# Optimization experiments

Hardware: AMD Instinct MI355X
Metric: run time of the kernel (lower is better)

The kernel has to match this reference:

```python
import jax, jax.numpy as jnp
import numpy as np

NE = 256          # number of electrons
D = 256           # attention_dim = num_heads * heads_dim
H = 4             # num_heads
DH = 64           # heads_dim
L = 2             # num_layers
NDETS = 1
MASK_LEN = 0.1


def _ln(x, s, b):
    m = jnp.mean(x, -1, keepdims=True)
    v = jnp.var(x, -1, keepdims=True)
    return (x - m) * jax.lax.rsqrt(v + 1e-5) * s + b


def setup_inputs() -> dict:
    key = jax.random.key(0)
    ks = jax.random.split(key, 16)
    n = lambda k, sh, sc: (jax.random.normal(k, sh) * sc).astype(jnp.float32)
    theta = jax.random.uniform(ks[0], (NE,), minval=0.1, maxval=np.pi - 0.1)
    phi = jax.random.uniform(ks[1], (NE,), minval=0.0, maxval=2.0 * np.pi)
    return {
        "electrons": jnp.stack([theta, phi], -1).astype(jnp.float32),
        "W_in": n(ks[2], (3, D), 3 ** -0.5),
        "Wq": n(ks[3], (L, D, H, DH), D ** -0.5),
        "bq": jnp.zeros((L, H, DH), jnp.float32),
        "Wk": n(ks[4], (L, D, H, DH), D ** -0.5),
        "bk": jnp.zeros((L, H, DH), jnp.float32),
        "Wv": n(ks[5], (L, D, H, DH), D ** -0.5),
        "bv": jnp.zeros((L, H, DH), jnp.float32),
        "Wo": n(ks[6], (L, H, DH, D), D ** -0.5),
        "bo": jnp.zeros((L, D), jnp.float32),
        "W1": n(ks[7], (L, D, D), D ** -0.5),
        "ln1_s": jnp.ones((L, D), jnp.float32),
        "ln1_b": jnp.zeros((L, D), jnp.float32),
        "W2": n(ks[8], (L, D, D), D ** -0.5),
        "b2": jnp.zeros((L, D), jnp.float32),
        "ln2_s": jnp.ones((L, D), jnp.float32),
        "ln2_b": jnp.zeros((L, D), jnp.float32),
        "Worb_r": n(ks[9], (D, NDETS * 2), D ** -0.5),
        "Worb_i": n(ks[10], (D, NDETS * 2), D ** -0.5),
    }


def reference(electrons, W_in, Wq, bq, Wk, bk, Wv, bv, Wo, bo, W1, ln1_s, ln1_b,
              W2, b2, ln2_s, ln2_b, Worb_r, Worb_i):
    theta, phi = electrons[..., 0], electrons[..., 1]
    # ---- pair gather: P = NE*(NE-1)/2 unordered pairs ----
    iu, ju = jnp.triu_indices(NE, k=1)
    th_p = jnp.stack([theta[iu], theta[ju]], -1)   # [P, 2]
    ph_p = jnp.stack([phi[iu], phi[ju]], -1)       # [P, 2]
    # input_feature: (cos t, sin t cos p, sin t sin p)
    feat = jnp.stack([jnp.cos(th_p), jnp.sin(th_p) * jnp.cos(ph_p),
                      jnp.sin(th_p) * jnp.sin(ph_p)], -1)  # [P, 2, 3]
    # ---- batched mini-transformer over all pairs (seq len 2) ----
    h = feat @ W_in  # [P, 2, D]
    for l in range(L):
        q = jnp.einsum('psd,dhk->pshk', h, Wq[l]) + bq[l]
        k = jnp.einsum('psd,dhk->pshk', h, Wk[l]) + bk[l]
        v = jnp.einsum('psd,dhk->pshk', h, Wv[l]) + bv[l]
        logits = jnp.einsum('pshk,pthk->phst', q / np.sqrt(DH), k)
        attn = jax.nn.softmax(logits, axis=-1)
        o = jnp.einsum('phst,pthk->pshk', attn, v)
        mha = jnp.einsum('pshk,hkd->psd', o, Wo[l]) + bo[l]
        h = h + mha @ W1[l]
        h = _ln(h, ln1_s[l], ln1_b[l])
        h = h + jnp.tanh(h @ W2[l] + b2[l])
        h = _ln(h, ln2_s[l], ln2_b[l])
    # ---- pair orbitals: complex dense -> [P, ndets, 2 elec, 2 orb] ----
    orb = (h @ Worb_r + 1j * (h @ Worb_i)).astype(jnp.complex64)  # [P, 2, ndets*2]
    orb = orb.reshape(-1, 2, NDETS, 2).transpose(0, 2, 1, 3)      # [P, ndets, 2, 2]
    # ---- pairwise truncation factor ----
    u = jnp.cos(th_p / 2) * jnp.exp(1j * ph_p / 2)   # [P, 2]
    v_ = jnp.sin(th_p / 2) * jnp.exp(-1j * ph_p / 2)
    chord = jnp.abs(u[:, 0] * v_[:, 1] - u[:, 1] * v_[:, 0])
    trunc = 1.0 - jnp.exp(-(chord / MASK_LEN) ** 2)  # [P]
    orb = orb * trunc[:, None, None, None]
    dets = jnp.linalg.det(orb)          # [P, ndets]
    pair_orbs = jnp.sum(dets, axis=-1)  # [P]
    # ---- scatter into antisymmetric NE x NE matrix ----
    pf = jnp.zeros((NE, NE), jnp.complex64).at[iu, ju].set(pair_orbs)
    pf = pf - pf.T
    # ---- cusp matrix ----
    ue = jnp.cos(theta / 2) * jnp.exp(0.5j * phi)   # [NE]
    ve = jnp.sin(theta / 2) * jnp.exp(-0.5j * phi)
    elem = ue[:, None] * ve[None, :] - ve[:, None] * ue[None, :]  # [NE, NE]
    eye = jnp.eye(NE, dtype=jnp.float32)
    elem_c = elem + eye
    rho_c = jnp.abs(elem_c)
    cusp = elem_c * jnp.exp(-(rho_c / MASK_LEN) ** 2)
    # ---- pfaffian = sqrt(det), in log space for stability ----
    sign, logabs = jnp.linalg.slogdet(pf + cusp)
    log_ferm = 0.5 * (logabs.astype(jnp.complex64) + 1j * jnp.angle(sign))
    # ---- bosonic flux attachment (truncated product), in log space ----
    rho = jnp.abs(elem)
    masked = jnp.sqrt(MASK_LEN ** 2 + rho ** 2) * elem / (rho + eye) + eye
    log_bos = jnp.sum(jnp.log(masked.astype(jnp.complex64)))
    return log_ferm + log_bos
```

## Files before the change

kernel.cpp:

```cpp
#include <hip/hip_runtime.h>
#include <math.h>
#include <stdint.h>

#define NE 256
#define DD 256
#define NL 2
#define P_TOT 32640
#define NCHUNK 3
#define PC (P_TOT / NCHUNK)
#define MC (2 * PC)
#define MT (MC / 128)
#define NB 32
#define NPANEL (NE / NB)

typedef __bf16 bf16x8 __attribute__((ext_vector_type(8)));
typedef float f32x4 __attribute__((ext_vector_type(4)));

__device__ __forceinline__ float bf2f(ushort h) {
    union { unsigned u; float f; } c; c.u = ((unsigned)h) << 16; return c.f;
}
__device__ __forceinline__ ushort f2bf(float f) {
    union { float f; unsigned u; } c; c.f = f;
    unsigned u = c.u;
    return (ushort)((u + 0x7fffu + ((u >> 16) & 1u)) >> 16);
}

#define GLD16(gp, lp) __builtin_amdgcn_global_load_lds( \
    (const __attribute__((address_space(1))) unsigned int*)(uintptr_t)(gp), \
    (__attribute__((address_space(3))) unsigned int*)(uintptr_t)(lp), 16, 0, 0)

__global__ void idx_k(int* __restrict__ ip, int* __restrict__ jp) {
    int i = threadIdx.x;
    int base = i * 255 - (i * (i - 1)) / 2;
    for (int j = i + 1; j < NE; ++j) {
        ip[base + j - i - 1] = i;
        jp[base + j - i - 1] = j;
    }
}

__global__ void zero_k(float* __restrict__ acc) {
    if (threadIdx.x < 8) acc[threadIdx.x] = 0.f;
}

__global__ __launch_bounds__(256) void prep_w_k(
    const float* __restrict__ Wq, const float* __restrict__ Wk, const float* __restrict__ Wv,
    const float* __restrict__ Wo, const float* __restrict__ W1, const float* __restrict__ W2,
    ushort* __restrict__ Wqkv_t, ushort* __restrict__ Woth_t) {
    __shared__ float Ts[32][33];
    int z = blockIdx.z, l = z / 6, m = z % 6;
    const float* src;
    ushort* dst;
    if (m == 0)      { src = Wq + l * 65536; dst = Wqkv_t + (size_t)l * 768 * 256 + 0 * 65536; }
    else if (m == 1) { src = Wk + l * 65536; dst = Wqkv_t + (size_t)l * 768 * 256 + 1 * 65536; }
    else if (m == 2) { src = Wv + l * 65536; dst = Wqkv_t + (size_t)l * 768 * 256 + 2 * 65536; }
    else             { src = (m == 3 ? Wo : m == 4 ? W1 : W2) + l * 65536;
                       dst = Woth_t + (size_t)(l * 3 + (m - 3)) * 65536; }
    int k0 = blockIdx.x * 32, n0 = blockIdx.y * 32;
    int t = threadIdx.x, tr = t >> 5, tc = t & 31;
    for (int i = tr; i < 32; i += 8) Ts[i][tc] = src[(size_t)(k0 + i) * 256 + n0 + tc];
    __syncthreads();
    for (int i = tr; i < 32; i += 8) dst[(size_t)(n0 + i) * 256 + k0 + tc] = f2bf(Ts[tc][i]);
}

__global__ void prep_b_k(const float* __restrict__ bq, const float* __restrict__ bk,
                         const float* __restrict__ bv, float* __restrict__ bqkv) {
    int l = blockIdx.x, t = threadIdx.x;
    bqkv[l * 768 + t] = bq[l * 256 + t];
    bqkv[l * 768 + 256 + t] = bk[l * 256 + t];
    bqkv[l * 768 + 512 + t] = bv[l * 256 + t];
}

__global__ __launch_bounds__(256) void embed_k(
    const float* __restrict__ el, const float* __restrict__ Win,
    const int* __restrict__ ip, const int* __restrict__ jp,
    ushort* __restrict__ h, int P0) {
    int w = threadIdx.x >> 6, lane = threadIdx.x & 63;
    int r = blockIdx.x * 4 + w;
    int gp = P0 + (r >> 1);
    int e = (r & 1) ? jp[gp] : ip[gp];
    float th = el[2 * e], ph = el[2 * e + 1];
    float st = sinf(th);
    float f0 = cosf(th), f1 = st * cosf(ph), f2 = st * sinf(ph);
    int n = lane * 4;
    float4 w0 = *(const float4*)&Win[n];
    float4 w1 = *(const float4*)&Win[256 + n];
    float4 w2 = *(const float4*)&Win[512 + n];
    ushort4 o;
    o.x = f2bf(f0 * w0.x + f1 * w1.x + f2 * w2.x);
    o.y = f2bf(f0 * w0.y + f1 * w1.y + f2 * w2.y);
    o.z = f2bf(f0 * w0.z + f1 * w1.z + f2 * w2.z);
    o.w = f2bf(f0 * w0.w + f1 * w1.w + f2 * w2.w);
    *(ushort4*)&h[(size_t)r * 256 + n] = o;
}

template <bool BIAS, bool RES>
__global__ __launch_bounds__(256) void gemm_k(
    const ushort* __restrict__ A, int lda,
    const ushort* __restrict__ Bt,
    const float* __restrict__ bias,
    const ushort* __restrict__ Rm, int ldr,
    ushort* __restrict__ C, int ldc) {
    __shared__ ushort As[128 * 64];
    __shared__ ushort Bs[128 * 64];
    int t = threadIdx.x, lane = t & 63, w = t >> 6;
    int row0 = blockIdx.x * 128, col0 = blockIdx.y * 128;
    int lrow = lane >> 3;
    int kx = ((lane & 7) ^ lrow) << 3;
    const ushort* gA = A + (size_t)(row0 + w * 32 + lrow) * lda + kx;
    const ushort* gB = Bt + (size_t)(col0 + w * 32 + lrow) * 256 + kx;
    f32x4 acc[4][4];
#pragma unroll
    for (int i = 0; i < 4; ++i)
#pragma unroll
        for (int j = 0; j < 4; ++j) acc[i][j] = (f32x4){0.f, 0.f, 0.f, 0.f};
    int wm = w >> 1, wn = w & 1;
    int mbase = wm * 64 + (lane & 15);
    int nbase = wn * 64 + (lane & 15);
    int l7 = lane & 7;
    for (int k0 = 0; k0 < 256; k0 += 64) {
        __syncthreads();
#pragma unroll
        for (int c2 = 0; c2 < 4; ++c2) {
            GLD16(gA + (size_t)(c2 * 8) * lda + k0, &As[(w * 4 + c2) * 512]);
            GLD16(gB + (size_t)(c2 * 8) * 256 + k0, &Bs[(w * 4 + c2) * 512]);
        }
        __syncthreads();
#pragma unroll
        for (int ks = 0; ks < 2; ++ks) {
            int kb = ks * 4 + (lane >> 4);
            bf16x8 af[4], bfr[4];
#pragma unroll
            for (int tm = 0; tm < 4; ++tm)
                af[tm] = *(const bf16x8*)&As[(mbase + tm * 16) * 64 + ((kb ^ l7) << 3)];
#pragma unroll
            for (int tn = 0; tn < 4; ++tn)
                bfr[tn] = *(const bf16x8*)&Bs[(nbase + tn * 16) * 64 + ((kb ^ l7) << 3)];
#pragma unroll
            for (int tm = 0; tm < 4; ++tm)
#pragma unroll
                for (int tn = 0; tn < 4; ++tn)
                    acc[tm][tn] = __builtin_amdgcn_mfma_f32_16x16x32_bf16(
                        af[tm], bfr[tn], acc[tm][tn], 0, 0, 0);
        }
    }
    int q = lane >> 4;
    int crow = row0 + wm * 64 + q * 4;
    int ccol = col0 + wn * 64 + (lane & 15);
#pragma unroll
    for (int tm = 0; tm < 4; ++tm)
#pragma unroll
        for (int r = 0; r < 4; ++r) {
            int row = crow + tm * 16 + r;
#pragma unroll
            for (int tn = 0; tn < 4; ++tn) {
                int col = ccol + tn * 16;
                float v = acc[tm][tn][r];
                if (BIAS) v += bias[col];
                if (RES) v += bf2f(Rm[(size_t)row * ldr + col]);
                C[(size_t)row * ldc + col] = f2bf(v);
            }
        }
}

__global__ __launch_bounds__(256) void attn_k(ushort* __restrict__ qkv) {
    int wid = threadIdx.x >> 6, lane = threadIdx.x & 63;
    int gw = blockIdx.x * 4 + wid;
    int p = gw >> 2, hh = gw & 3;
    size_t r0 = (size_t)(2 * p) * 768 + hh * 64 + lane;
    size_t r1 = r0 + 768;
    float q0 = bf2f(qkv[r0]) * 0.125f, q1 = bf2f(qkv[r1]) * 0.125f;
    float k0 = bf2f(qkv[r0 + 256]), k1 = bf2f(qkv[r1 + 256]);
    float v0 = bf2f(qkv[r0 + 512]), v1 = bf2f(qkv[r1 + 512]);
    float s00 = q0 * k0, s01 = q0 * k1, s10 = q1 * k0, s11 = q1 * k1;
#pragma unroll
    for (int off = 32; off; off >>= 1) {
        s00 += __shfl_xor(s00, off, 64);
        s01 += __shfl_xor(s01, off, 64);
        s10 += __shfl_xor(s10, off, 64);
        s11 += __shfl_xor(s11, off, 64);
    }
    float m0 = fmaxf(s00, s01), m1 = fmaxf(s10, s11);
    float e00 = expf(s00 - m0), e01 = expf(s01 - m0);
    float e10 = expf(s10 - m1), e11 = expf(s11 - m1);
    float i0 = 1.f / (e00 + e01), i1 = 1.f / (e10 + e11);
    float o0 = (e00 * i0) * v0 + (e01 * i0) * v1;
    float o1 = (e10 * i1) * v0 + (e11 * i1) * v1;
    qkv[r0] = f2bf(o0);
    qkv[r1] = f2bf(o1);
}

__global__ __launch_bounds__(256) void ln_a_k(
    const ushort* __restrict__ X, int ldx, ushort* __restrict__ H,
    const float* __restrict__ sc, const float* __restrict__ bi) {
    int w = threadIdx.x >> 6, lane = threadIdx.x & 63;
    int r = blockIdx.x * 4 + w;
    int d0 = lane * 4;
    ushort4 xv = *(const ushort4*)&X[(size_t)r * ldx + d0];
    float x[4] = {bf2f(xv.x), bf2f(xv.y), bf2f(xv.z), bf2f(xv.w)};
    float sum = x[0] + x[1] + x[2] + x[3];
    float sq = x[0] * x[0] + x[1] * x[1] + x[2] * x[2] + x[3] * x[3];
#pragma unroll
    for (int off = 32; off; off >>= 1) {
        sum += __shfl_xor(sum, off, 64);
        sq += __shfl_xor(sq, off, 64);
    }
    float m = sum * (1.f / 256.f);
    float var = sq * (1.f / 256.f) - m * m;
    float rs = rsqrtf(var + 1e-5f);
    float4 s4 = *(const float4*)&sc[d0];
    float4 b4 = *(const float4*)&bi[d0];
    ushort4 o;
    o.x = f2bf((x[0] - m) * rs * s4.x + b4.x);
    o.y = f2bf((x[1] - m) * rs * s4.y + b4.y);
    o.z = f2bf((x[2] - m) * rs * s4.z + b4.z);
    o.w = f2bf((x[3] - m) * rs * s4.w + b4.w);
    *(ushort4*)&H[(size_t)r * 256 + d0] = o;
}

__global__ __launch_bounds__(256) void ln_b_k(
    ushort* __restrict__ H, const ushort* __restrict__ T,
    const float* __restrict__ sc, const float* __restrict__ bi) {
    int w = threadIdx.x >> 6, lane = threadIdx.x & 63;
    int r = blockIdx.x * 4 + w;
    int d0 = lane * 4;
    ushort4 hv = *(const ushort4*)&H[(size_t)r * 256 + d0];
    ushort4 tv = *(const ushort4*)&T[(size_t)r * 256 + d0];
    float x[4];
    x[0] = bf2f(hv.x) + tanhf(bf2f(tv.x));
    x[1] = bf2f(hv.y) + tanhf(bf2f(tv.y));
    x[2] = bf2f(hv.z) + tanhf(bf2f(tv.z));
    x[3] = bf2f(hv.w) + tanhf(bf2f(tv.w));
    float sum = x[0] + x[1] + x[2] + x[3];
    float sq = x[0] * x[0] + x[1] * x[1] + x[2] * x[2] + x[3] * x[3];
#pragma unroll
    for (int off = 32; off; off >>= 1) {
        sum += __shfl_xor(sum, off, 64);
        sq += __shfl_xor(sq, off, 64);
    }
    float m = sum * (1.f / 256.f);
    float var = sq * (1.f / 256.f) - m * m;
    float rs = rsqrtf(var + 1e-5f);
    float4 s4 = *(const float4*)&sc[d0];
    float4 b4 = *(const float4*)&bi[d0];
    ushort4 o;
    o.x = f2bf((x[0] - m) * rs * s4.x + b4.x);
    o.y = f2bf((x[1] - m) * rs * s4.y + b4.y);
    o.z = f2bf((x[2] - m) * rs * s4.z + b4.z);
    o.w = f2bf((x[3] - m) * rs * s4.w + b4.w);
    *(ushort4*)&H[(size_t)r * 256 + d0] = o;
}

__global__ __launch_bounds__(256) void orb_k(
    const ushort* __restrict__ h, const float* __restrict__ Wr, const float* __restrict__ Wi,
    const float* __restrict__ el, const int* __restrict__ ip, const int* __restrict__ jp,
    float2* __restrict__ porb, int P0) {
    int w = threadIdx.x >> 6, lane = threadIdx.x & 63;
    int p = blockIdx.x * 4 + w;
    const ushort* h0 = h + (size_t)(2 * p) * 256;
    int d0 = lane * 4;
    ushort4 a0 = *(const ushort4*)&h0[d0];
    ushort4 a1 = *(const ushort4*)&h0[256 + d0];
    float x0[4] = {bf2f(a0.x), bf2f(a0.y), bf2f(a0.z), bf2f(a0.w)};
    float x1[4] = {bf2f(a1.x), bf2f(a1.y), bf2f(a1.z), bf2f(a1.w)};
    float wrv[8], wiv[8];
    *(float4*)&wrv[0] = *(const float4*)&Wr[2 * d0];
    *(float4*)&wrv[4] = *(const float4*)&Wr[2 * d0 + 4];
    *(float4*)&wiv[0] = *(const float4*)&Wi[2 * d0];
    *(float4*)&wiv[4] = *(const float4*)&Wi[2 * d0 + 4];
    float s[8] = {0, 0, 0, 0, 0, 0, 0, 0};
#pragma unroll
    for (int u = 0; u < 4; ++u) {
        s[0] += x0[u] * wrv[2 * u];     s[1] += x0[u] * wiv[2 * u];
        s[2] += x0[u] * wrv[2 * u + 1]; s[3] += x0[u] * wiv[2 * u + 1];
        s[4] += x1[u] * wrv[2 * u];     s[5] += x1[u] * wiv[2 * u];
        s[6] += x1[u] * wrv[2 * u + 1]; s[7] += x1[u] * wiv[2 * u + 1];
    }
#pragma unroll
    for (int off = 32; off; off >>= 1) {
#pragma unroll
        for (int q2 = 0; q2 < 8; ++q2) s[q2] += __shfl_xor(s[q2], off, 64);
    }
    if (lane == 0) {
        int gp = P0 + p;
        int i = ip[gp], j = jp[gp];
        float thi = el[2 * i], phi_ = el[2 * i + 1];
        float thj = el[2 * j], phj = el[2 * j + 1];
        float chi = cosf(thi * 0.5f), shi = sinf(thi * 0.5f);
        float chj = cosf(thj * 0.5f), shj = sinf(thj * 0.5f);
        float cpi = cosf(phi_ * 0.5f), spi = sinf(phi_ * 0.5f);
        float cpj = cosf(phj * 0.5f), spj = sinf(phj * 0.5f);
        float uix = chi * cpi, uiy = chi * spi;
        float vix = shi * cpi, viy = -shi * spi;
        float ujx = chj * cpj, ujy = chj * spj;
        float vjx = shj * cpj, vjy = -shj * spj;
        float crx = (uix * vjx - uiy * vjy) - (ujx * vix - ujy * viy);
        float cry = (uix * vjy + uiy * vjx) - (ujx * viy + ujy * vix);
        float chord2 = crx * crx + cry * cry;
        float trunc = 1.f - expf(-100.f * chord2);
        float t2 = trunc * trunc;
        float dr = (s[0] * s[6] - s[1] * s[7]) - (s[2] * s[4] - s[3] * s[5]);
        float di = (s[0] * s[7] + s[1] * s[6]) - (s[2] * s[5] + s[3] * s[4]);
        porb[gp] = make_float2(dr * t2, di * t2);
    }
}

__global__ __launch_bounds__(256) void assemble_k(
    const float* __restrict__ el, const float2* __restrict__ porb,
    float2* __restrict__ Am, float* acc) {
    __shared__ float sre[256], sim[256];
    int idx = blockIdx.x * 256 + threadIdx.x;
    int i = idx >> 8, j = idx & 255;
    float thi = el[2 * i], phi_ = el[2 * i + 1];
    float thj = el[2 * j], phj = el[2 * j + 1];
    float chi = cosf(thi * 0.5f), shi = sinf(thi * 0.5f);
    float chj = cosf(thj * 0.5f), shj = sinf(thj * 0.5f);
    float cpi = cosf(phi_ * 0.5f), spi = sinf(phi_ * 0.5f);
    float cpj = cosf(phj * 0.5f), spj = sinf(phj * 0.5f);
    float uix = chi * cpi, uiy = chi * spi;
    float vix = shi * cpi, viy = -shi * spi;
    float ujx = chj * cpj, ujy = chj * spj;
    float vjx = shj * cpj, vjy = -shj * spj;
    float ex = (uix * vjx - uiy * vjy) - (ujx * vix - ujy * viy);
    float ey = (uix * vjy + uiy * vjx) - (ujx * viy + ujy * vix);
    float pfx = 0.f, pfy = 0.f;
    if (i < j) {
        int pp = i * 255 - (i * (i - 1)) / 2 + (j - i - 1);
        float2 t = porb[pp]; pfx = t.x; pfy = t.y;
    } else if (i > j) {
        int pp = j * 255 - (j * (j - 1)) / 2 + (i - j - 1);
        float2 t = porb[pp]; pfx = -t.x; pfy = -t.y;
    }
    float eye = (i == j) ? 1.f : 0.f;
    float ecx = ex + eye, ecy = ey;
    float wgt = expf(-100.f * (ecx * ecx + ecy * ecy));
    Am[idx] = make_float2(pfx + ecx * wgt, pfy + ecy * wgt);
    float lre = 0.f, lim = 0.f;
    if (i != j) {
        float r2 = ex * ex + ey * ey;
        lre = 0.5f * logf(0.01f + r2);
        lim = atan2f(ey, ex);
    }
    sre[threadIdx.x] = lre; sim[threadIdx.x] = lim;
    __syncthreads();
    for (int s2 = 128; s2; s2 >>= 1) {
        if (threadIdx.x < s2) {
            sre[threadIdx.x] += sre[threadIdx.x + s2];
            sim[threadIdx.x] += sim[threadIdx.x + s2];
        }
        __syncthreads();
    }
    if (threadIdx.x == 0) {
        atomicAdd(acc + 0, sre[0]);
        atomicAdd(acc + 1, sim[0]);
    }
}

__device__ __forceinline__ unsigned wave_max_u32_dpp(unsigned m) {
#define DPP_STEP(ctrl) { \
    unsigned tmp_ = (unsigned)__builtin_amdgcn_update_dpp((int)m, (int)m, ctrl, 0xf, 0xf, false); \
    m = (m >= tmp_) ? m : tmp_; }
    DPP_STEP(0x111)
    DPP_STEP(0x112)
    DPP_STEP(0x114)
    DPP_STEP(0x118)
    DPP_STEP(0x142)
    DPP_STEP(0x143)
#undef DPP_STEP
    return (unsigned)__builtin_amdgcn_readlane((int)m, 63);
}

__global__ __launch_bounds__(256) void panel_k(
    float2* __restrict__ Am, int* __restrict__ pivg, float* __restrict__ acc, int k0) {
    __shared__ float2 Pn[NB][NE];
    __shared__ alignas(16) unsigned rbest4[2][4];
    __shared__ float2 diag_s[NB];
    int t = threadIdx.x, lane = t & 63, w = t >> 6;
    int nr = NE - k0;
    bool act = t < nr;
    float2 cur = make_float2(0.f, 0.f);
    if (act) {
        const float4* src = (const float4*)(Am + (size_t)(k0 + t) * NE + k0);
#pragma unroll
        for (int c2 = 0; c2 < NB / 2; ++c2) {
            float4 v = src[c2];
            Pn[2 * c2][t]     = make_float2(v.x, v.y);
            Pn[2 * c2 + 1][t] = make_float2(v.z, v.w);
            if (c2 == 0) cur = make_float2(v.x, v.y);
        }
    }
    __syncthreads();
    int lg = t;
    int nsw = 0;
#pragma unroll
    for (int j = 0; j < NB; ++j) {
        const int par = j & 1;
        unsigned pk = 0u;
        if (act && lg >= j) {
            float fv = fabsf(cur.x) + fabsf(cur.y);
            union { float f; unsigned u; } cu; cu.f = fv;
            pk = (cu.u & 0xFFFF0000u) | ((unsigned)lg << 8) | (unsigned)t;
        }
        unsigned wbest = wave_max_u32_dpp(pk);
        if (lane == 0) rbest4[par][w] = wbest;
        __syncthreads();
        uint4 rb = *(const uint4*)&rbest4[par][0];
        unsigned ga = rb.x >= rb.y ? rb.x : rb.y;
        unsigned gb = rb.z >= rb.w ? rb.z : rb.w;
        unsigned gg = ga >= gb ? ga : gb;
        int w_phys = (int)(gg & 255u);
        int l_w    = (int)((gg >> 8) & 255u);
        float2 d = Pn[j][w_phys];
        if (t == 0) {
            diag_s[j] = d;
            pivg[j] = k0 + l_w;
            if (l_w != j) nsw++;
        }
        int oldlg = lg;
        if (t == w_phys) lg = j;
        else if (oldlg == j) lg = l_w;
        float ivn = 1.f / (d.x * d.x + d.y * d.y);
        float inx = d.x * ivn, iny = -d.y * ivn;
        if (act && lg > j) {
            float2 L = make_float2(cur.x * inx - cur.y * iny,
                                   cur.x * iny + cur.y * inx);
            Pn[j][t] = L;
            float2 nxt = cur;
#pragma unroll
            for (int c = j + 1; c < NB; ++c) {
                float2 u = Pn[c][w_phys];
                float2 v = Pn[c][t];
                v.x -= L.x * u.x - L.y * u.y;
                v.y -= L.x * u.y + L.y * u.x;
                Pn[c][t] = v;
                if (c == j + 1) nxt = v;
            }
            cur = nxt;
        }
    }
    if (act) {
        float4* dst = (float4*)(Am + (size_t)(k0 + lg) * NE + k0);
#pragma unroll
        for (int c2 = 0; c2 < NB / 2; ++c2) {
            float2 e0 = Pn[2 * c2][t], e1 = Pn[2 * c2 + 1][t];
            dst[c2] = make_float4(e0.x, e0.y, e1.x, e1.y);
        }
    }
    __syncthreads();
    if (w == 0) {
        float lre = 0.f, lim = 0.f;
        if (lane < NB) {
            float2 d = diag_s[lane];
            lre = 0.5f * logf(d.x * d.x + d.y * d.y);
            lim = atan2f(d.y, d.x);
        }
#pragma unroll
        for (int off = 32; off; off >>= 1) {
            lre += __shfl_xor(lre, off, 64);
            lim += __shfl_xor(lim, off, 64);
        }
        if (lane == 0) { acc[2] += lre; acc[3] += lim; }
    }
    if (t == 0) acc[4] += (float)nsw;
}

__global__ __launch_bounds__(256) void trsm_k(
    float2* __restrict__ Am, const int* __restrict__ pivg, int k0) {
    __shared__ float2 Ls[NB][NB + 1];
    __shared__ short sigma[NE];
    __shared__ short rlist[NB];
    __shared__ int rcount;
    int t = threadIdx.x;
    sigma[t] = (short)t;
    for (int idx = t; idx < NB * NB; idx += 256)
        Ls[idx >> 5][idx & 31] = Am[(size_t)(k0 + (idx >> 5)) * NE + k0 + (idx & 31)];
    if (t < NB) rlist[t] = (short)k0;
    __syncthreads();
    if (t == 0) {
        for (int j = 0; j < NB; ++j) {
            int p = pivg[j], r1 = k0 + j;
            short tmp = sigma[r1]; sigma[r1] = sigma[p]; sigma[p] = tmp;
        }
        int cnt = 0;
        for (int r = k0 + NB; r < NE; ++r)
            if (sigma[r] != r) rlist[cnt++] = (short)r;
        rcount = cnt;
    }
    __syncthreads();
    int ncols = NE - k0 - NB;
    if (t >= ncols) return;
    int col = k0 + NB + t;
    int cnt = rcount;
    float2 x[NB];
#pragma unroll
    for (int i = 0; i < NB; ++i)
        x[i] = Am[(size_t)sigma[k0 + i] * NE + col];
    float2 extra[NB];
#pragma unroll
    for (int q = 0; q < NB; ++q)
        extra[q] = Am[(size_t)sigma[rlist[q]] * NE + col];
#pragma unroll
    for (int i = 1; i < NB; ++i) {
        float2 xi = x[i];
#pragma unroll
        for (int j = 0; j < i; ++j) {
            float2 l = Ls[i][j];
            xi.x -= l.x * x[j].x - l.y * x[j].y;
            xi.y -= l.x * x[j].y + l.y * x[j].x;
        }
        x[i] = xi;
    }
#pragma unroll
    for (int i = 0; i < NB; ++i)
        Am[(size_t)(k0 + i) * NE + col] = x[i];
#pragma unroll
    for (int q = 0; q < NB; ++q)
        if (q < cnt) Am[(size_t)rlist[q] * NE + col] = extra[q];
}

__global__ __launch_bounds__(256) void update_k(float2* __restrict__ Am, int k0) {
    __shared__ float2 Lt[NB][NB + 1];
    __shared__ float2 Ut[NB][NB + 1];
    int t = threadIdx.x;
    int r0 = k0 + NB + blockIdx.x * NB;
    int c0 = k0 + NB + blockIdx.y * NB;
    for (int idx = t; idx < NB * NB; idx += 256) {
        int a = idx >> 5, b = idx & 31;
        Lt[a][b] = Am[(size_t)(r0 + a) * NE + k0 + b];
        Ut[a][b] = Am[(size_t)(k0 + a) * NE + c0 + b];
    }
    __syncthreads();
    int lr = t >> 3, lc0 = (t & 7) * 4;
    float2 s0 = {0.f, 0.f}, s1 = {0.f, 0.f}, s2 = {0.f, 0.f}, s3 = {0.f, 0.f};
#pragma unroll
    for (int k = 0; k < NB; ++k) {
        float2 a = Lt[lr][k];
        float2 u0 = Ut[k][lc0 + 0], u1 = Ut[k][lc0 + 1];
        float2 u2 = Ut[k][lc0 + 2], u3 = Ut[k][lc0 + 3];
        s0.x += a.x * u0.x - a.y * u0.y; s0.y += a.x * u0.y + a.y * u0.x;
        s1.x += a.x * u1.x - a.y * u1.y; s1.y += a.x * u1.y + a.y * u1.x;
        s2.x += a.x * u2.x - a.y * u2.y; s2.y += a.x * u2.y + a.y * u2.x;
        s3.x += a.x * u3.x - a.y * u3.y; s3.y += a.x * u3.y + a.y * u3.x;
    }
    size_t base = (size_t)(r0 + lr) * NE + c0 + lc0;
    float2 cc;
    cc = Am[base + 0]; cc.x -= s0.x; cc.y -= s0.y; Am[base + 0] = cc;
    cc = Am[base + 1]; cc.x -= s1.x; cc.y -= s1.y; Am[base + 1] = cc;
    cc = Am[base + 2]; cc.x -= s2.x; cc.y -= s2.y; Am[base + 2] = cc;
    cc = Am[base + 3]; cc.x -= s3.x; cc.y -= s3.y; Am[base + 3] = cc;
}

__global__ void finalize_k(const float* __restrict__ acc, float* __restrict__ out) {
    if (threadIdx.x == 0) {
        float ang = acc[3] + 3.14159265358979323846f * acc[4];
        ang -= 6.283185307179586f * rintf(ang * 0.15915494309189535f);
        out[0] = 0.5f * acc[2] + acc[0];
        out[1] = 0.5f * ang + acc[1];
    }
}

extern "C" void kernel_launch(void* const* d_in, const int* in_sizes, int n_in,
                              void* d_out, int out_size, void* d_ws, size_t ws_size,
                              hipStream_t stream) {
    (void)in_sizes; (void)n_in; (void)out_size;
    const float* el   = (const float*)d_in[0];
    const float* Win  = (const float*)d_in[1];
    const float* Wq   = (const float*)d_in[2];
    const float* bq   = (const float*)d_in[3];
    const float* Wk   = (const float*)d_in[4];
    const float* bk   = (const float*)d_in[5];
    const float* Wv   = (const float*)d_in[6];
    const float* bv   = (const float*)d_in[7];
    const float* Wo   = (const float*)d_in[8];
    const float* bo   = (const float*)d_in[9];
    const float* W1   = (const float*)d_in[10];
    const float* ln1s = (const float*)d_in[11];
    const float* ln1b = (const float*)d_in[12];
    const float* W2   = (const float*)d_in[13];
    const float* b2   = (const float*)d_in[14];
    const float* ln2s = (const float*)d_in[15];
    const float* ln2b = (const float*)d_in[16];
    const float* Wor  = (const float*)d_in[17];
    const float* Woi  = (const float*)d_in[18];

    char* wp = (char*)d_ws;
    auto alloc = [&](size_t b) {
        char* r = wp;
        wp += (b + 255) & ~(size_t)255;
        return r;
    };
    int*    ipb  = (int*)alloc((size_t)P_TOT * 4);
    int*    jpb  = (int*)alloc((size_t)P_TOT * 4);
    float2* porb = (float2*)alloc((size_t)P_TOT * 8);
    float2* Am   = (float2*)alloc((size_t)NE * NE * 8);
    float*  acc  = (float*)alloc(256);
    int*    pivg = (int*)alloc((size_t)NE * 4);
    ushort* Wqkv_t = (ushort*)alloc((size_t)2 * 768 * 256 * 2);
    ushort* Woth_t = (ushort*)alloc((size_t)6 * 65536 * 2);
    float*  bqkv = (float*)alloc((size_t)2 * 768 * 4);
    ushort* hb   = (ushort*)alloc((size_t)MC * 256 * 2);
    ushort* qkvb = (ushort*)alloc((size_t)MC * 768 * 2);
    ushort* tb   = (ushort*)alloc((size_t)MC * 256 * 2);
    size_t need = (size_t)(wp - (char*)d_ws);
    if (need > ws_size) {
        zero_k<<<1, 64, 0, stream>>>((float*)d_out);
        return;
    }

    prep_w_k<<<dim3(8, 8, 12), 256, 0, stream>>>(Wq, Wk, Wv, Wo, W1, W2, Wqkv_t, Woth_t);
    prep_b_k<<<2, 256, 0, stream>>>(bq, bk, bv, bqkv);
    idx_k<<<1, 256, 0, stream>>>(ipb, jpb);
    zero_k<<<1, 64, 0, stream>>>(acc);

    for (int c = 0; c < NCHUNK; ++c) {
        int P0 = c * PC;
        embed_k<<<MC / 4, 256, 0, stream>>>(el, Win, ipb, jpb, hb, P0);
        for (int l = 0; l < NL; ++l) {
            gemm_k<true, false><<<dim3(MT, 6), 256, 0, stream>>>(
                hb, 256, Wqkv_t + (size_t)l * 768 * 256, bqkv + l * 768, nullptr, 0, qkvb, 768);
            attn_k<<<PC, 256, 0, stream>>>(qkvb);
            gemm_k<true, false><<<dim3(MT, 2), 256, 0, stream>>>(
                qkvb, 768, Woth_t + (size_t)(l * 3 + 0) * 65536, bo + l * 256, nullptr, 0, tb, 256);
            gemm_k<false, true><<<dim3(MT, 2), 256, 0, stream>>>(
                tb, 256, Woth_t + (size_t)(l * 3 + 1) * 65536, nullptr, hb, 256, qkvb, 768);
            ln_a_k<<<MC / 4, 256, 0, stream>>>(qkvb, 768, hb, ln1s + l * 256, ln1b + l * 256);
            gemm_k<true, false><<<dim3(MT, 2), 256, 0, stream>>>(
                hb, 256, Woth_t + (size_t)(l * 3 + 2) * 65536, b2 + l * 256, nullptr, 0, tb, 256);
            ln_b_k<<<MC / 4, 256, 0, stream>>>(hb, tb, ln2s + l * 256, ln2b + l * 256);
        }
        orb_k<<<PC / 4, 256, 0, stream>>>(hb, Wor, Woi, el, ipb, jpb, porb, P0);
    }
    assemble_k<<<NE, 256, 0, stream>>>(el, porb, Am, acc);

    for (int p = 0; p < NPANEL; ++p) {
        int k0 = p * NB;
        panel_k<<<1, 256, 0, stream>>>(Am, pivg + p * NB, acc, k0);
        int m = NE - k0 - NB;
        if (m > 0) {
            trsm_k<<<1, 256, 0, stream>>>(Am, pivg + p * NB, k0);
            dim3 ug(m / NB, m / NB);
            update_k<<<ug, 256, 0, stream>>>(Am, k0);
        }
    }
    finalize_k<<<1, 64, 0, stream>>>(acc, (float*)d_out);
}
```

Baseline: 1.161 ms.

## Fold Wo into W1, pick chunk count from workspace, and restructure panel pivot loop

Precomputes a fused Wo·W1 weight and bias so the attention output projection and the first MLP matmul become one GEMM with a residual epilogue, removing a full GEMM and an intermediate buffer pass per layer. It also chooses the fewest pair chunks that fit in the workspace, which cuts kernel launches and gives larger grids. The panel LU kernel stops unrolling its outer loop, buffers pivots in shared memory, and uses a fixed-length masked inner loop. Folding the two projections changes rounding, since the product is stored in bf16, and this is only valid if nothing nonlinear sits between Wo and W1.

```diff
diff --git a/kernel.cpp b/kernel.cpp
--- a/kernel.cpp
+++ b/kernel.cpp
@@ -6,10 +6,6 @@
 #define DD 256
 #define NL 2
 #define P_TOT 32640
-#define NCHUNK 3
-#define PC (P_TOT / NCHUNK)
-#define MC (2 * PC)
-#define MT (MC / 128)
 #define NB 32
 #define NPANEL (NE / NB)
 
@@ -68,6 +64,47 @@
     bqkv[l * 768 + t] = bq[l * 256 + t];
     bqkv[l * 768 + 256 + t] = bk[l * 256 + t];
     bqkv[l * 768 + 512 + t] = bv[l * 256 + t];
+}
+
+__global__ __launch_bounds__(256) void fuse_w_k(
+    const float* __restrict__ Wo, const float* __restrict__ W1,
+    ushort* __restrict__ Wf_t) {
+    __shared__ float WoS[32][33];
+    __shared__ float W1S[32][33];
+    int l = blockIdx.z;
+    int n0 = blockIdx.x * 32, d0 = blockIdx.y * 32;
+    const float* wo = Wo + l * 65536;
+    const float* w1 = W1 + l * 65536;
+    int t = threadIdx.x, ty = t >> 5, tx = t & 31;
+    float acc4[4] = {0.f, 0.f, 0.f, 0.f};
+    for (int m0 = 0; m0 < 256; m0 += 32) {
+        __syncthreads();
+        for (int i = ty; i < 32; i += 8) {
+            WoS[i][tx] = wo[(size_t)(d0 + i) * 256 + m0 + tx];
+            W1S[i][tx] = w1[(size_t)(m0 + i) * 256 + n0 + tx];
+        }
+        __syncthreads();
+#pragma unroll
+        for (int jm = 0; jm < 32; ++jm) {
+            float a = WoS[tx][jm];
+#pragma unroll
+            for (int q = 0; q < 4; ++q)
+                acc4[q] += a * W1S[jm][ty + 8 * q];
+        }
+    }
+#pragma unroll
+    for (int q = 0; q < 4; ++q)
+        Wf_t[(size_t)l * 65536 + (size_t)(n0 + ty + 8 * q) * 256 + d0 + tx] = f2bf(acc4[q]);
+}
+
+__global__ void fuse_b_k(const float* __restrict__ bo, const float* __restrict__ W1,
+                         float* __restrict__ bfuse) {
+    int l = blockIdx.x, n = threadIdx.x;
+    const float* w1 = W1 + l * 65536;
+    const float* b = bo + l * 256;
+    float s = 0.f;
+    for (int m = 0; m < 256; ++m) s += b[m] * w1[(size_t)m * 256 + n];
+    bfuse[l * 256 + n] = s;
 }
 
 __global__ __launch_bounds__(256) void embed_k(
@@ -374,6 +411,7 @@
     __shared__ float2 Pn[NB][NE];
     __shared__ alignas(16) unsigned rbest4[2][4];
     __shared__ float2 diag_s[NB];
+    __shared__ short piv_s[NB];
     int t = threadIdx.x, lane = t & 63, w = t >> 6;
     int nr = NE - k0;
     bool act = t < nr;
@@ -391,7 +429,6 @@
     __syncthreads();
     int lg = t;
     int nsw = 0;
-#pragma unroll
     for (int j = 0; j < NB; ++j) {
         const int par = j & 1;
         unsigned pk = 0u;
@@ -412,7 +449,7 @@
         float2 d = Pn[j][w_phys];
         if (t == 0) {
             diag_s[j] = d;
-            pivg[j] = k0 + l_w;
+            piv_s[j] = (short)l_w;
             if (l_w != j) nsw++;
         }
         int oldlg = lg;
@@ -426,11 +463,14 @@
             Pn[j][t] = L;
             float2 nxt = cur;
 #pragma unroll
-            for (int c = j + 1; c < NB; ++c) {
+            for (int c = 0; c < NB; ++c) {
                 float2 u = Pn[c][w_phys];
                 float2 v = Pn[c][t];
-                v.x -= L.x * u.x - L.y * u.y;
-                v.y -= L.x * u.y + L.y * u.x;
+                bool en = c > j;
+                float ux = en ? u.x : 0.f;
+                float uy = en ? u.y : 0.f;
+                v.x -= L.x * ux - L.y * uy;
+                v.y -= L.x * uy + L.y * ux;
                 Pn[c][t] = v;
                 if (c == j + 1) nxt = v;
             }
@@ -446,6 +486,7 @@
         }
     }
     __syncthreads();
+    if (t < NB) pivg[t] = k0 + (int)piv_s[t];
     if (w == 0) {
         float lre = 0.f, lim = 0.f;
         if (lane < NB) {
@@ -596,38 +637,53 @@
     int*    pivg = (int*)alloc((size_t)NE * 4);
     ushort* Wqkv_t = (ushort*)alloc((size_t)2 * 768 * 256 * 2);
     ushort* Woth_t = (ushort*)alloc((size_t)6 * 65536 * 2);
+    ushort* Wf_t   = (ushort*)alloc((size_t)2 * 65536 * 2);
+    float*  bfuse  = (float*)alloc((size_t)2 * 256 * 4);
     float*  bqkv = (float*)alloc((size_t)2 * 768 * 4);
-    ushort* hb   = (ushort*)alloc((size_t)MC * 256 * 2);
-    ushort* qkvb = (ushort*)alloc((size_t)MC * 768 * 2);
-    ushort* tb   = (ushort*)alloc((size_t)MC * 256 * 2);
-    size_t need = (size_t)(wp - (char*)d_ws);
-    if (need > ws_size) {
+    size_t fixed = (size_t)(wp - (char*)d_ws);
+
+    int nchunk = 0, PCr = 0, MCr = 0;
+    const int cands[3] = {1, 2, 3};
+    for (int ci = 0; ci < 3; ++ci) {
+        int pc = P_TOT / cands[ci];
+        size_t mc = (size_t)2 * pc;
+        size_t var = 0;
+        var += ((mc * 256 * 2 + 255) & ~(size_t)255);
+        var += ((mc * 768 * 2 + 255) & ~(size_t)255);
+        var += ((mc * 256 * 2 + 255) & ~(size_t)255);
+        if (fixed + var <= ws_size) { nchunk = cands[ci]; PCr = pc; MCr = (int)mc; break; }
+    }
+    if (!nchunk) {
         zero_k<<<1, 64, 0, stream>>>((float*)d_out);
         return;
     }
+    ushort* hb   = (ushort*)alloc((size_t)MCr * 256 * 2);
+    ushort* qkvb = (ushort*)alloc((size_t)MCr * 768 * 2);
+    ushort* tb   = (ushort*)alloc((size_t)MCr * 256 * 2);
+    int MTr = MCr / 128;
 
     prep_w_k<<<dim3(8, 8, 12), 256, 0, stream>>>(Wq, Wk, Wv, Wo, W1, W2, Wqkv_t, Woth_t);
     prep_b_k<<<2, 256, 0, stream>>>(bq, bk, bv, bqkv);
+    fuse_w_k<<<dim3(8, 8, 2), 256, 0, stream>>>(Wo, W1, Wf_t);
+    fuse_b_k<<<2, 256, 0, stream>>>(bo, W1, bfuse);
     idx_k<<<1, 256, 0, stream>>>(ipb, jpb);
     zero_k<<<1, 64, 0, stream>>>(acc);
 
-    for (int c = 0; c < NCHUNK; ++c) {
-        int P0 = c * PC;
-        embed_k<<<MC / 4, 256, 0, stream>>>(el, Win, ipb, jpb, hb, P0);
+    for (int c = 0; c < nchunk; ++c) {
+        int P0 = c * PCr;
+        embed_k<<<MCr / 4, 256, 0, stream>>>(el, Win, ipb, jpb, hb, P0);
         for (int l = 0; l < NL; ++l) {
-            gemm_k<true, false><<<dim3(MT, 6), 256, 0, stream>>>(
+            gemm_k<true, false><<<dim3(MTr, 6), 256, 0, stream>>>(
                 hb, 256, Wqkv_t + (size_t)l * 768 * 256, bqkv + l * 768, nullptr, 0, qkvb, 768);
-            attn_k<<<PC, 256, 0, stream>>>(qkvb);
-            gemm_k<true, false><<<dim3(MT, 2), 256, 0, stream>>>(
-                qkvb, 768, Woth_t + (size_t)(l * 3 + 0) * 65536, bo + l * 256, nullptr, 0, tb, 256);
-            gemm_k<false, true><<<dim3(MT, 2), 256, 0, stream>>>(
-                tb, 256, Woth_t + (size_t)(l * 3 + 1) * 65536, nullptr, hb, 256, qkvb, 768);
-            ln_a_k<<<MC / 4, 256, 0, stream>>>(qkvb, 768, hb, ln1s + l * 256, ln1b + l * 256);
-            gemm_k<true, false><<<dim3(MT, 2), 256, 0, stream>>>(
+            attn_k<<<PCr, 256, 0, stream>>>(qkvb);
+            gemm_k<true, true><<<dim3(MTr, 2), 256, 0, stream>>>(
+                qkvb, 768, Wf_t + (size_t)l * 65536, bfuse + l * 256, hb, 256, tb, 256);
+            ln_a_k<<<MCr / 4, 256, 0, stream>>>(tb, 256, hb, ln1s + l * 256, ln1b + l * 256);
+            gemm_k<true, false><<<dim3(MTr, 2), 256, 0, stream>>>(
                 hb, 256, Woth_t + (size_t)(l * 3 + 2) * 65536, b2 + l * 256, nullptr, 0, tb, 256);
-            ln_b_k<<<MC / 4, 256, 0, stream>>>(hb, tb, ln2s + l * 256, ln2b + l * 256);
-        }
-        orb_k<<<PC / 4, 256, 0, stream>>>(hb, Wor, Woi, el, ipb, jpb, porb, P0);
+            ln_b_k<<<MCr / 4, 256, 0, stream>>>(hb, tb, ln2s + l * 256, ln2b + l * 256);
+        }
+        orb_k<<<PCr / 4, 256, 0, stream>>>(hb, Wor, Woi, el, ipb, jpb, porb, P0);
     }
     assemble_k<<<NE, 256, 0, stream>>>(el, porb, Am, acc);
 
```

Result: slower. 1.290 ms (+11.1%).
